# Kernel optimization log

Measured on AMD Instinct MI355X. Metric: run time of the kernel, lower is better.

## Reference

```python
import jax, jax.numpy as jnp
import numpy as np

B, N, D_IN, D_OUT, R = 8, 2048, 256, 256, 4


def setup_inputs() -> dict:
    key = jax.random.key(0)
    k1, k2, k3, k4 = jax.random.split(key, 4)
    x = jax.random.normal(k1, (B, N, D_IN), dtype=jnp.float32)
    adj = jnp.zeros((1,), dtype=jnp.float32)  # unused by the module
    # relation-type matrix: 0 = no edge, 1..R = relation id
    relation = jax.random.randint(k2, (B, N, N), 0, R + 1, dtype=jnp.int32)
    weight = jax.random.normal(k3, (R, D_IN, D_OUT), dtype=jnp.float32) * 0.05
    bias = jax.random.normal(k4, (D_OUT,), dtype=jnp.float32) * 0.05
    return {"x": x, "adj": adj, "relation": relation, "weight": weight, "bias": bias}


def reference(x, adj, relation, weight, bias):
    # Binary per-relation adjacency masks: [R, B, N, N]
    rel_ids = jnp.arange(1, weight.shape[0] + 1, dtype=relation.dtype)
    masks = (relation[None] == rel_ids[:, None, None, None]).astype(x.dtype)
    # Aggregate neighbors per relation: h[r] = A_r @ x  -> [R, B, N, D_in]
    h = jnp.einsum('rbnm,bmd->rbnd', masks, x)
    # Per-relation output transform, summed over relations: [B, N, D_out]
    y = jnp.einsum('rbnd,rdo->bno', h, weight)
    return y + bias
```

## Files before the change

kernel.cpp:

```cpp
#include <hip/hip_runtime.h>
#include <hip/hip_bf16.h>
#include <stdint.h>

typedef uint32_t u32;
typedef uint64_t u64;
typedef __bf16 bf16x8 __attribute__((ext_vector_type(8)));
typedef float f32x4 __attribute__((ext_vector_type(4)));
typedef u32 u32x4 __attribute__((ext_vector_type(4)));

#define NB 8
#define NN 2048
#define DIN 256
#define DOUT 256
#define NR 4
#define KTOT (NN * NR)

#define XW_BYTES   (NB * DOUT * KTOT * 2)
#define PART_BYTES (NB * NN * DOUT * 4)
#define WT_BYTES   (NR * DIN * DOUT * 2)
#define PART_ELEMS (NB * NN * DOUT)

__device__ __forceinline__ ushort f2bf(float f) {
  union { float f; u32 u; } c; c.f = f;
  return (ushort)((c.u + 0x7FFFu + ((c.u >> 16) & 1u)) >> 16);
}

__device__ __forceinline__ float bf2f(ushort u) {
  union { u32 i; float f; } c; c.i = ((u32)u) << 16; return c.f;
}

__device__ __forceinline__ void gload_lds16(const void* g, void* l) {
  __builtin_amdgcn_global_load_lds(
      (const __attribute__((address_space(1))) u32*)g,
      (__attribute__((address_space(3))) u32*)l, 16, 0, 0);
}

__global__ void k0_wT(const float* __restrict__ w, ushort* __restrict__ wT) {
  int i = blockIdx.x * 256 + threadIdx.x;
  int o = i & 255, d = (i >> 8) & 255, r = i >> 16;
  wT[(r * DOUT + o) * DIN + d] = f2bf(w[i]);
}

__global__ __launch_bounds__(512) void k1_xw(const float* __restrict__ x,
                                             const ushort* __restrict__ wT,
                                             ushort* __restrict__ xwT) {
  __shared__ char smem[73728];
  char* const Ab0 = smem;
  char* const Ab1 = smem + 4096;
  char* const Bb0 = smem + 8192;
  char* const Bb1 = smem + 40960;
  const int t = threadIdx.x, l = t & 63, w = t >> 6;
  const int r = w >> 1, oh = w & 1;
  const int blk = blockIdx.x;
  const int b = blk >> 6, rest = blk & 63, mc = rest >> 1, ot = rest & 1;

  f32x4 acc[4][4] = {};
  const int fr = l & 15, fq = l >> 4;
  const int ru = ((fq ^ (fr & 3)) << 4);

  const int arow = t >> 3;
  const int abyte = ((((t & 7) >> 1) ^ (arow & 3)) << 4) + (t & 1) * 8;
  const float* xg = x + ((size_t)(b * NN + mc * 64 + arow) * DIN + (t & 7) * 4);

  const int bdd = (((t & 3) ^ ((t >> 2) & 3)) << 3);
  const int bro = (t >> 2);

#define K1_GLDB(D0, BB)                                                        \
  {                                                                            \
    _Pragma("unroll") for (int i = 0; i < 4; ++i) {                            \
      const ushort* src = wT + ((size_t)(i * DOUT + ot * 128 + bro) * DIN +    \
                                (D0) + bdd);                                   \
      gload_lds16(src, (BB) + i * 8192 + t * 16);                              \
    }                                                                          \
  }

#define K1_WRA(AB, XV)                                                         \
  {                                                                            \
    ushort4 a4;                                                                \
    a4.x = f2bf((XV).x); a4.y = f2bf((XV).y);                                  \
    a4.z = f2bf((XV).z); a4.w = f2bf((XV).w);                                  \
    *(ushort4*)((AB) + arow * 64 + abyte) = a4;                                \
  }

#define K1_MFMA(AB, BB)                                                        \
  {                                                                            \
    bf16x8 af[4];                                                              \
    __builtin_amdgcn_s_setprio(1);                                             \
    _Pragma("unroll") for (int fm = 0; fm < 4; ++fm)                           \
      af[fm] = *(const bf16x8*)((AB) + (fm * 16 + fr) * 64 + ru);              \
    _Pragma("unroll") for (int fo = 0; fo < 4; ++fo) {                         \
      bf16x8 bf = *(const bf16x8*)((BB) + (size_t)(r * 128 + oh * 64 +         \
                                   fo * 16 + fr) * 64 + ru);                   \
      _Pragma("unroll") for (int fm = 0; fm < 4; ++fm)                         \
        acc[fm][fo] = __builtin_amdgcn_mfma_f32_16x16x32_bf16(                 \
            af[fm], bf, acc[fm][fo], 0, 0, 0);                                 \
    }                                                                          \
    __builtin_amdgcn_s_setprio(0);                                             \
  }

#define K1_ENDF()                                                              \
  asm volatile("s_waitcnt vmcnt(0) lgkmcnt(0)" ::: "memory");                  \
  __builtin_amdgcn_s_barrier();                                                \
  __builtin_amdgcn_sched_barrier(0);

#define K1_STEP(S, AP, BP, AQ, BQ)                                             \
  {                                                                            \
    K1_GLDB((S + 1) * 32, BQ);                                                 \
    __builtin_amdgcn_sched_barrier(0);                                         \
    float4 xv = *(const float4*)(xg + (S + 1) * 32);                           \
    K1_MFMA(AP, BP);                                                           \
    K1_WRA(AQ, xv);                                                            \
    K1_ENDF();                                                                 \
  }

  K1_GLDB(0, Bb0);
  __builtin_amdgcn_sched_barrier(0);
  {
    float4 xv = *(const float4*)(xg);
    K1_WRA(Ab0, xv);
  }
  K1_ENDF();

  K1_STEP(0, Ab0, Bb0, Ab1, Bb1);
  K1_STEP(1, Ab1, Bb1, Ab0, Bb0);
  K1_STEP(2, Ab0, Bb0, Ab1, Bb1);
  K1_STEP(3, Ab1, Bb1, Ab0, Bb0);
  K1_STEP(4, Ab0, Bb0, Ab1, Bb1);
  K1_STEP(5, Ab1, Bb1, Ab0, Bb0);
  K1_STEP(6, Ab0, Bb0, Ab1, Bb1);
  K1_MFMA(Ab1, Bb1);
  __syncthreads();

  ushort* Cs = (ushort*)smem;
#pragma unroll
  for (int fm = 0; fm < 4; ++fm)
#pragma unroll
    for (int fo = 0; fo < 4; ++fo)
#pragma unroll
      for (int j = 0; j < 4; ++j) {
        int o_loc = oh * 64 + fo * 16 + fr;
        int ml = fm * 16 + fq * 4 + j;
        Cs[o_loc * 256 + ml * 4 + r] = f2bf(acc[fm][fo][j]);
      }
  __syncthreads();
#pragma unroll
  for (int i = 0; i < 8; ++i) {
    int el = (i * 512 + t) * 8;
    int o_loc = el >> 8, kp = el & 255;
    *(uint4*)(xwT + (size_t)(b * DOUT + ot * 128 + o_loc) * KTOT + mc * 256 + kp) =
        *(const uint4*)(Cs + el);
  }
#undef K1_STEP
#undef K1_ENDF
#undef K1_MFMA
#undef K1_WRA
#undef K1_GLDB
}

__global__ __launch_bounds__(512, 2) void k2_v2(const int* __restrict__ rel,
                                                const ushort* __restrict__ xwT,
                                                ushort* __restrict__ partb) {
  __shared__ char smem[131072];
  const int t = threadIdx.x, l = t & 63, w = t >> 6;
  const int wm = w >> 2, wn = w & 3;
  const int logical = (blockIdx.x & 7) * 32 + (blockIdx.x >> 3);
  const int b = logical >> 5;
  const int nt = (logical >> 2) & 7;
  const int ks = logical & 3;

  f32x4 acc[8][4] = {};
  const int fr = l & 15, fq = l >> 4;
  const int rswz = (fr & 7) << 4;

  char* const Ab0 = smem;
  char* const Ab1 = smem + 32768;
  char* const Bb0 = smem + 65536;
  char* const Bb1 = smem + 98304;

  const int arow = t >> 1, half = t & 1;
  const int aswz = (arow & 7) << 4;
  const int* relg = rel + ((size_t)(b * NN + nt * 256 + arow)) * NN + ks * 512 + half * 8;

  const int brow = t >> 3;
  const int kd = (((t & 7) ^ ((t >> 3) & 7)) << 3);
  const ushort* xwb = xwT + (size_t)b * DOUT * KTOT + ks * 2048;

  int4 rs0a, rs0b, rs1a, rs1b;

#define GLD_ALL(S, BB)                                                         \
  {                                                                            \
    _Pragma("unroll") for (int i = 0; i < 4; ++i)                              \
      gload_lds16(xwb + (size_t)(brow + 64 * i) * KTOT + (S) * 64 + kd,        \
                  (BB) + i * 8192 + t * 16);                                   \
  }

#define RELLOAD(S, RA, RB)                                                     \
  RA = *(const int4*)(relg + (S) * 16);                                        \
  RB = *(const int4*)(relg + (S) * 16 + 4);

#define EXPAND_A(ABASE, V0, V1)                                                \
  {                                                                            \
    char* rowp = (ABASE) + arow * 128;                                         \
    int vv[8] = {V0.x, V0.y, V0.z, V0.w, V1.x, V1.y, V1.z, V1.w};              \
    _Pragma("unroll") for (int p = 0; p < 4; ++p) {                            \
      int va = vv[2 * p], vb = vv[2 * p + 1];                                  \
      u32 sa = ((u32)(va - 1) & 3u) * 16u;                                     \
      u32 sb = ((u32)(vb - 1) & 3u) * 16u;                                     \
      u64 ha = va ? (0x3F80ull << sa) : 0ull;                                  \
      u64 hb = vb ? (0x3F80ull << sb) : 0ull;                                  \
      u32x4 e = {(u32)ha, (u32)(ha >> 32), (u32)hb, (u32)(hb >> 32)};          \
      *(u32x4*)(rowp + ((half * 64 + p * 16) ^ aswz)) = e;                     \
    }                                                                          \
  }

#define RDB(BV, BB, KK)                                                        \
  _Pragma("unroll") for (int fo = 0; fo < 4; ++fo)                             \
    BV[fo] = *(const bf16x8*)((BB) + (wn * 64 + fo * 16 + fr) * 128 +          \
                              (((KK) * 64 + fq * 16) ^ rswz));

#define RDA(AV, AB, FM0, KK)                                                   \
  _Pragma("unroll") for (int i = 0; i < 4; ++i)                                \
    AV[i] = *(const bf16x8*)((AB) + (wm * 128 + ((FM0) + i) * 16 + fr) * 128 + \
                             (((KK) * 64 + fq * 16) ^ rswz));

#define MFMA4(FM0, AV, BV)                                                     \
  __builtin_amdgcn_s_setprio(1);                                               \
  _Pragma("unroll") for (int i = 0; i < 4; ++i)                                \
    _Pragma("unroll") for (int fo = 0; fo < 4; ++fo)                           \
      acc[(FM0) + i][fo] = __builtin_amdgcn_mfma_f32_16x16x32_bf16(            \
          AV[i], BV[fo], acc[(FM0) + i][fo], 0, 0, 0);                         \
  __builtin_amdgcn_s_setprio(0);

#define ENDFENCE(VMS)                                                          \
  asm volatile("s_waitcnt vmcnt(" VMS ") lgkmcnt(0)" ::: "memory");            \
  __builtin_amdgcn_s_barrier();                                                \
  __builtin_amdgcn_sched_barrier(0);

#define STEP(S, P, Q, STG, REL, EXP, VMS)                                      \
  {                                                                            \
    bf16x8 b0[4], b1[4], aA[4], aB[4], aC[4], aD[4];                           \
    RDB(b0, Bb##P, 0);                                                         \
    RDA(aA, Ab##P, 0, 0);                                                      \
    if (STG) { GLD_ALL((S) + 1, Bb##Q); }                                      \
    __builtin_amdgcn_sched_barrier(0);                                         \
    if (REL) { RELLOAD((S) + 2, rs##P##a, rs##P##b); }                         \
    RDA(aB, Ab##P, 4, 0);                                                      \
    MFMA4(0, aA, b0);                                                          \
    RDA(aC, Ab##P, 0, 1);                                                      \
    if (EXP) { EXPAND_A(Ab##Q, rs##Q##a, rs##Q##b); }                          \
    MFMA4(4, aB, b0);                                                          \
    RDB(b1, Bb##P, 1);                                                         \
    RDA(aD, Ab##P, 4, 1);                                                      \
    MFMA4(0, aC, b1);                                                          \
    MFMA4(4, aD, b1);                                                          \
    ENDFENCE(VMS);                                                             \
  }

  GLD_ALL(0, Bb0);
  __builtin_amdgcn_sched_barrier(0);
  RELLOAD(0, rs0a, rs0b);
  RELLOAD(1, rs1a, rs1b);
  EXPAND_A(Ab0, rs0a, rs0b);
  ENDFENCE("4");

  for (int s = 0; s < 30; s += 2) {
    STEP(s, 0, 1, 1, 1, 1, "2");
    STEP(s + 1, 1, 0, 1, 1, 1, "2");
  }
  STEP(30, 0, 1, 1, 0, 1, "0");
  {
    bf16x8 b0[4], b1[4], aA[4], aB[4], aC[4], aD[4];
    RDB(b0, Bb1, 0);
    RDA(aA, Ab1, 0, 0);
    RDA(aB, Ab1, 4, 0);
    MFMA4(0, aA, b0);
    RDA(aC, Ab1, 0, 1);
    MFMA4(4, aB, b0);
    RDB(b1, Bb1, 1);
    RDA(aD, Ab1, 4, 1);
    MFMA4(0, aC, b1);
    MFMA4(4, aD, b1);
  }

  ushort* dst = partb + (size_t)ks * PART_ELEMS;
#pragma unroll
  for (int fm = 0; fm < 8; ++fm)
#pragma unroll
    for (int fo = 0; fo < 4; ++fo) {
      int n = nt * 256 + wm * 128 + fm * 16 + fq * 4;
      int o = wn * 64 + fo * 16 + fr;
#pragma unroll
      for (int j = 0; j < 4; ++j)
        dst[(size_t)(b * NN + n + j) * DOUT + o] = f2bf(acc[fm][fo][j]);
    }
#undef STEP
#undef ENDFENCE
#undef MFMA4
#undef RDA
#undef RDB
#undef EXPAND_A
#undef RELLOAD
#undef GLD_ALL
}

__global__ void k3_sum(float* __restrict__ out, const ushort* __restrict__ partb,
                       const float* __restrict__ bias) {
  int i = blockIdx.x * 256 + threadIdx.x;
  float4 s = ((const float4*)bias)[i & 63];
#pragma unroll
  for (int p = 0; p < 4; ++p) {
    ushort4 v = ((const ushort4*)(partb + (size_t)p * PART_ELEMS))[i];
    s.x += bf2f(v.x); s.y += bf2f(v.y); s.z += bf2f(v.z); s.w += bf2f(v.w);
  }
  ((float4*)out)[i] = s;
}

__global__ __launch_bounds__(256, 2) void k2_r4(const int* __restrict__ rel,
                                                const ushort* __restrict__ xwT,
                                                float* __restrict__ out,
                                                float* __restrict__ part) {
  __shared__ char smem[81920];
  const int t = threadIdx.x, l = t & 63, w = t >> 6;
  const int wr = w >> 1, wc = w & 1;
  const int logical = (blockIdx.x & 7) * 64 + (blockIdx.x >> 3);
  const int b = logical >> 6;
  const int nt = (logical >> 2) & 15;
  const int ks = (logical >> 1) & 1;
  const int ot = logical & 1;

  f32x4 acc[4][4] = {};
  const int arow = t >> 1, half = t & 1;
  const int* relg = rel + ((size_t)(b * NN + nt * 128 + arow) * NN + ks * 1024 + half * 8);
  const ushort* xwb = xwT + (size_t)(b * DOUT + ot * 128) * KTOT + ks * 4096;

  char* const Ab0 = smem;
  char* const Ab1 = smem + 16384;
  char* const Bb0 = smem + 32768;
  char* const Bb1 = smem + 49152;
  char* const Bb2 = smem + 65536;

  const int brow = t >> 3;
  const int kd = (((t & 7) ^ ((t >> 3) & 7)) << 3);
  const int aswz = (arow & 7) << 4;
  const int fr = l & 15, fq = l >> 4;
  const int rswz = (fr & 7) << 4;

  int4 rsA0, rsB0, rsA1, rsB1;

#define STAGE_B(S, BBASE)                                                      \
  {                                                                            \
    _Pragma("unroll") for (int i = 0; i < 4; ++i)                              \
      gload_lds16(xwb + (size_t)(brow + 32 * i) * KTOT + (S) * 64 + kd,        \
                  (BBASE) + i * 4096 + t * 16);                                \
  }
#define RELLOAD(S, RA, RB)                                                     \
  RA = *(const int4*)(relg + (S) * 16);                                        \
  RB = *(const int4*)(relg + (S) * 16 + 4);
#define EXPAND_A(ABASE, V0, V1)                                                \
  {                                                                            \
    char* rowp = (ABASE) + arow * 128;                                         \
    int vv[8] = {V0.x, V0.y, V0.z, V0.w, V1.x, V1.y, V1.z, V1.w};              \
    _Pragma("unroll") for (int p = 0; p < 4; ++p) {                            \
      int va = vv[2 * p], vb = vv[2 * p + 1];                                  \
      u32 sa = ((u32)(va - 1) & 3u) * 16u;                                     \
      u32 sb = ((u32)(vb - 1) & 3u) * 16u;                                     \
      u64 ha = va ? (0x3F80ull << sa) : 0ull;                                  \
      u64 hb = vb ? (0x3F80ull << sb) : 0ull;                                  \
      u32x4 e = {(u32)ha, (u32)(ha >> 32), (u32)hb, (u32)(hb >> 32)};          \
      *(u32x4*)(rowp + ((half * 64 + p * 16) ^ aswz)) = e;                     \
    }                                                                          \
  }
#define BARV6()                                                                \
  asm volatile("s_waitcnt vmcnt(6) lgkmcnt(0)" ::: "memory");                  \
  __builtin_amdgcn_s_barrier();                                                \
  __builtin_amdgcn_sched_barrier(0);
#define BARV0()                                                                \
  asm volatile("s_waitcnt vmcnt(0) lgkmcnt(0)" ::: "memory");                  \
  __builtin_amdgcn_s_barrier();                                                \
  __builtin_amdgcn_sched_barrier(0);
#define MFMA_STEP(AC, BC)                                                      \
  __builtin_amdgcn_s_setprio(1);                                               \
  _Pragma("unroll") for (int kk = 0; kk < 2; ++kk) {                           \
    bf16x8 af[4], bfv[4];                                                      \
    const int colb = (kk * 64 + fq * 16) ^ rswz;                               \
    _Pragma("unroll") for (int fm = 0; fm < 4; ++fm)                           \
      af[fm] = *(const bf16x8*)((AC) + (wr * 64 + fm * 16 + fr) * 128 + colb); \
    _Pragma("unroll") for (int fo = 0; fo < 4; ++fo)                           \
      bfv[fo] = *(const bf16x8*)((BC) + (wc * 64 + fo * 16 + fr) * 128 + colb);\
    _Pragma("unroll") for (int fm = 0; fm < 4; ++fm)                           \
      _Pragma("unroll") for (int fo = 0; fo < 4; ++fo)                         \
        acc[fm][fo] = __builtin_amdgcn_mfma_f32_16x16x32_bf16(                 \
            af[fm], bfv[fo], acc[fm][fo], 0, 0, 0);                            \
  }                                                                            \
  __builtin_amdgcn_s_setprio(0);
#define BODY(S, ACUR, BCUR, ANXT, RLA, RLB, RCA, RCB, BSTG)                    \
  {                                                                            \
    STAGE_B((S) + 2, BSTG);                                                    \
    RELLOAD((S) + 2, RLA, RLB);                                                \
    MFMA_STEP(ACUR, BCUR);                                                     \
    EXPAND_A(ANXT, RCA, RCB);                                                  \
    BARV6();                                                                   \
  }

  STAGE_B(0, Bb0);
  RELLOAD(0, rsA0, rsB0);
  STAGE_B(1, Bb1);
  RELLOAD(1, rsA1, rsB1);
  EXPAND_A(Ab0, rsA0, rsB0);
  BARV6();

  for (int s = 0; s < 60; s += 6) {
    BODY(s + 0, Ab0, Bb0, Ab1, rsA0, rsB0, rsA1, rsB1, Bb2);
    BODY(s + 1, Ab1, Bb1, Ab0, rsA1, rsB1, rsA0, rsB0, Bb0);
    BODY(s + 2, Ab0, Bb2, Ab1, rsA0, rsB0, rsA1, rsB1, Bb1);
    BODY(s + 3, Ab1, Bb0, Ab0, rsA1, rsB1, rsA0, rsB0, Bb2);
    BODY(s + 4, Ab0, Bb1, Ab1, rsA0, rsB0, rsA1, rsB1, Bb0);
    BODY(s + 5, Ab1, Bb2, Ab0, rsA1, rsB1, rsA0, rsB0, Bb1);
  }
  BODY(60, Ab0, Bb0, Ab1, rsA0, rsB0, rsA1, rsB1, Bb2);
  BODY(61, Ab1, Bb1, Ab0, rsA1, rsB1, rsA0, rsB0, Bb0);
  {
    MFMA_STEP(Ab0, Bb2);
    EXPAND_A(Ab1, rsA1, rsB1);
    BARV0();
  }
  {
    MFMA_STEP(Ab1, Bb0);
  }

  float* dst = ks ? part : out;
#pragma unroll
  for (int fm = 0; fm < 4; ++fm)
#pragma unroll
    for (int fo = 0; fo < 4; ++fo) {
      int n = nt * 128 + wr * 64 + fm * 16 + fq * 4;
      int o = ot * 128 + wc * 64 + fo * 16 + fr;
#pragma unroll
      for (int j = 0; j < 4; ++j)
        dst[(size_t)(b * NN + n + j) * DOUT + o] = acc[fm][fo][j];
    }
#undef BODY
#undef MFMA_STEP
#undef BARV6
#undef BARV0
#undef EXPAND_A
#undef RELLOAD
#undef STAGE_B
}

__global__ void k3_r4(float* __restrict__ out, const float* __restrict__ part,
                      const float* __restrict__ bias) {
  int i = blockIdx.x * 256 + threadIdx.x;
  float4 o = ((const float4*)out)[i];
  float4 p = ((const float4*)part)[i];
  float4 bv = ((const float4*)bias)[i & 63];
  float4 rr;
  rr.x = o.x + p.x + bv.x;
  rr.y = o.y + p.y + bv.y;
  rr.z = o.z + p.z + bv.z;
  rr.w = o.w + p.w + bv.w;
  ((float4*)out)[i] = rr;
}

extern "C" void kernel_launch(void* const* d_in, const int* in_sizes, int n_in,
                              void* d_out, int out_size, void* d_ws, size_t ws_size,
                              hipStream_t stream) {
  const float* x = (const float*)d_in[0];
  const int* rel = (const int*)d_in[2];
  const float* wgt = (const float*)d_in[3];
  const float* bias = (const float*)d_in[4];
  float* out = (float*)d_out;
  char* ws = (char*)d_ws;

  const size_t partb_bytes = (size_t)PART_ELEMS * 2 * 4;
  const size_t need_big = (size_t)XW_BYTES + partb_bytes + WT_BYTES;
  if (ws_size >= need_big) {
    ushort* xwT = (ushort*)ws;
    ushort* partb = (ushort*)(ws + XW_BYTES);
    ushort* wT = (ushort*)(ws + XW_BYTES + partb_bytes);
    k0_wT<<<1024, 256, 0, stream>>>(wgt, wT);
    k1_xw<<<512, 512, 0, stream>>>(x, wT, xwT);
    k2_v2<<<256, 512, 0, stream>>>(rel, xwT, partb);
    k3_sum<<<4096, 256, 0, stream>>>(out, partb, bias);
  } else {
    ushort* xwT = (ushort*)ws;
    float* part = (float*)(ws + XW_BYTES);
    ushort* wT = (ushort*)(ws + XW_BYTES + PART_BYTES);
    k0_wT<<<1024, 256, 0, stream>>>(wgt, wT);
    k1_xw<<<512, 512, 0, stream>>>(x, wT, xwT);
    k2_r4<<<512, 256, 0, stream>>>(rel, xwT, out, part);
    k3_r4<<<4096, 256, 0, stream>>>(out, part, bias);
  }
}
```

Measured before the change: 108.4 us.

## Retile relation GEMM to 256x128 tiles with 32-wide K steps for higher occupancy

The main aggregation kernel is retiled. Each block now computes a 256-row by 128-column output tile instead of 256x256, and the K step shrinks from 64 to 32, so LDS per block drops from 128KB to 48KB. The grid doubles to 512 blocks with launch bounds allowing 4 blocks per CU, and the LDS swizzle is redone for 64-byte rows. The aim is more resident waves and better latency hiding. The cost is that the relation matrix is read and expanded twice (once per output half), and there are twice as many barriers per unit of K.

```diff
diff --git a/kernel.cpp b/kernel.cpp
--- a/kernel.cpp
+++ b/kernel.cpp
@@ -157,150 +157,133 @@
 #undef K1_GLDB
 }
 
-__global__ __launch_bounds__(512, 2) void k2_v2(const int* __restrict__ rel,
+__global__ __launch_bounds__(512, 4) void k2_v7(const int* __restrict__ rel,
                                                 const ushort* __restrict__ xwT,
                                                 ushort* __restrict__ partb) {
-  __shared__ char smem[131072];
+  __shared__ char smem[49152];
   const int t = threadIdx.x, l = t & 63, w = t >> 6;
-  const int wm = w >> 2, wn = w & 3;
-  const int logical = (blockIdx.x & 7) * 32 + (blockIdx.x >> 3);
-  const int b = logical >> 5;
-  const int nt = (logical >> 2) & 7;
+  const int wm = w >> 1, wn = w & 1;
+  const int logical = (blockIdx.x & 7) * 64 + (blockIdx.x >> 3);
+  const int b = logical >> 6;
+  const int nt = (logical >> 3) & 7;
+  const int ot = (logical >> 2) & 1;
   const int ks = logical & 3;
 
-  f32x4 acc[8][4] = {};
+  f32x4 acc[4][4] = {};
   const int fr = l & 15, fq = l >> 4;
-  const int rswz = (fr & 7) << 4;
+  const int runit = ((fq ^ (fr & 3) ^ ((fr >> 2) & 3)) << 4);
 
   char* const Ab0 = smem;
-  char* const Ab1 = smem + 32768;
-  char* const Bb0 = smem + 65536;
-  char* const Bb1 = smem + 98304;
+  char* const Ab1 = smem + 16384;
+  char* const Bb0 = smem + 32768;
+  char* const Bb1 = smem + 40960;
 
   const int arow = t >> 1, half = t & 1;
-  const int aswz = (arow & 7) << 4;
-  const int* relg = rel + ((size_t)(b * NN + nt * 256 + arow)) * NN + ks * 512 + half * 8;
-
-  const int brow = t >> 3;
-  const int kd = (((t & 7) ^ ((t >> 3) & 7)) << 3);
-  const ushort* xwb = xwT + (size_t)b * DOUT * KTOT + ks * 2048;
-
-  int4 rs0a, rs0b, rs1a, rs1b;
-
-#define GLD_ALL(S, BB)                                                         \
-  {                                                                            \
-    _Pragma("unroll") for (int i = 0; i < 4; ++i)                              \
-      gload_lds16(xwb + (size_t)(brow + 64 * i) * KTOT + (S) * 64 + kd,        \
-                  (BB) + i * 8192 + t * 16);                                   \
-  }
-
-#define RELLOAD(S, RA, RB)                                                     \
-  RA = *(const int4*)(relg + (S) * 16);                                        \
-  RB = *(const int4*)(relg + (S) * 16 + 4);
-
-#define EXPAND_A(ABASE, V0, V1)                                                \
-  {                                                                            \
-    char* rowp = (ABASE) + arow * 128;                                         \
-    int vv[8] = {V0.x, V0.y, V0.z, V0.w, V1.x, V1.y, V1.z, V1.w};              \
-    _Pragma("unroll") for (int p = 0; p < 4; ++p) {                            \
-      int va = vv[2 * p], vb = vv[2 * p + 1];                                  \
-      u32 sa = ((u32)(va - 1) & 3u) * 16u;                                     \
-      u32 sb = ((u32)(vb - 1) & 3u) * 16u;                                     \
-      u64 ha = va ? (0x3F80ull << sa) : 0ull;                                  \
-      u64 hb = vb ? (0x3F80ull << sb) : 0ull;                                  \
-      u32x4 e = {(u32)ha, (u32)(ha >> 32), (u32)hb, (u32)(hb >> 32)};          \
-      *(u32x4*)(rowp + ((half * 64 + p * 16) ^ aswz)) = e;                     \
-    }                                                                          \
-  }
-
-#define RDB(BV, BB, KK)                                                        \
+  const int* relg = rel + ((size_t)(b * NN + nt * 256 + arow)) * NN + ks * 512 + half * 4;
+  const u32 awz = ((u32)arow & 3u) ^ (((u32)arow >> 2) & 3u);
+  char* const rowA0 = Ab0 + arow * 64;
+  char* const rowA1 = Ab1 + arow * 64;
+
+  const int brow = t >> 2;
+  const int bsw = (((t & 3) ^ ((brow & 3) ^ ((brow >> 2) & 3))) << 3);
+  const ushort* xwb = xwT + (size_t)(b * DOUT + ot * 128) * KTOT + ks * 2048;
+
+  int4 rs0, rs1;
+
+#define GLD_B(S, BB)                                                           \
+  gload_lds16(xwb + (size_t)brow * KTOT + (S) * 32 + bsw, (BB) + t * 16);
+
+#define RELLOAD(S, R) R = *(const int4*)(relg + (S) * 8);
+
+#define EXPROW(ROWP, V)                                                        \
+  {                                                                            \
+    u32 sa = ((u32)((V).x - 1) & 3u) * 16u, sb = ((u32)((V).y - 1) & 3u) * 16u;\
+    u32 sc = ((u32)((V).z - 1) & 3u) * 16u, sd = ((u32)((V).w - 1) & 3u) * 16u;\
+    u64 ha = (V).x ? (0x3F80ull << sa) : 0ull;                                 \
+    u64 hb = (V).y ? (0x3F80ull << sb) : 0ull;                                 \
+    u64 hc = (V).z ? (0x3F80ull << sc) : 0ull;                                 \
+    u64 hd = (V).w ? (0x3F80ull << sd) : 0ull;                                 \
+    u32x4 e0 = {(u32)ha, (u32)(ha >> 32), (u32)hb, (u32)(hb >> 32)};           \
+    u32x4 e1 = {(u32)hc, (u32)(hc >> 32), (u32)hd, (u32)(hd >> 32)};           \
+    *(u32x4*)((ROWP) + ((((u32)(half * 2 + 0)) ^ awz) << 4)) = e0;             \
+    *(u32x4*)((ROWP) + ((((u32)(half * 2 + 1)) ^ awz) << 4)) = e1;             \
+  }
+
+#define RDA(AV, AB)                                                            \
+  _Pragma("unroll") for (int fm = 0; fm < 4; ++fm)                             \
+    AV[fm] = *(const bf16x8*)((AB) + (wm * 64 + fm * 16 + fr) * 64 + runit);
+
+#define RDB(BV, BB)                                                            \
   _Pragma("unroll") for (int fo = 0; fo < 4; ++fo)                             \
-    BV[fo] = *(const bf16x8*)((BB) + (wn * 64 + fo * 16 + fr) * 128 +          \
-                              (((KK) * 64 + fq * 16) ^ rswz));
-
-#define RDA(AV, AB, FM0, KK)                                                   \
-  _Pragma("unroll") for (int i = 0; i < 4; ++i)                                \
-    AV[i] = *(const bf16x8*)((AB) + (wm * 128 + ((FM0) + i) * 16 + fr) * 128 + \
-                             (((KK) * 64 + fq * 16) ^ rswz));
-
-#define MFMA4(FM0, AV, BV)                                                     \
+    BV[fo] = *(const bf16x8*)((BB) + (wn * 64 + fo * 16 + fr) * 64 + runit);
+
+#define MFMA2(FM0, AV, BV)                                                     \
   __builtin_amdgcn_s_setprio(1);                                               \
-  _Pragma("unroll") for (int i = 0; i < 4; ++i)                                \
+  _Pragma("unroll") for (int i = 0; i < 2; ++i)                                \
     _Pragma("unroll") for (int fo = 0; fo < 4; ++fo)                           \
       acc[(FM0) + i][fo] = __builtin_amdgcn_mfma_f32_16x16x32_bf16(            \
-          AV[i], BV[fo], acc[(FM0) + i][fo], 0, 0, 0);                         \
+          AV[(FM0) + i], BV[fo], acc[(FM0) + i][fo], 0, 0, 0);                 \
   __builtin_amdgcn_s_setprio(0);
 
-#define ENDFENCE(VMS)                                                          \
+#define ENDF(VMS)                                                              \
   asm volatile("s_waitcnt vmcnt(" VMS ") lgkmcnt(0)" ::: "memory");            \
   __builtin_amdgcn_s_barrier();                                                \
   __builtin_amdgcn_sched_barrier(0);
 
 #define STEP(S, P, Q, STG, REL, EXP, VMS)                                      \
   {                                                                            \
-    bf16x8 b0[4], b1[4], aA[4], aB[4], aC[4], aD[4];                           \
-    RDB(b0, Bb##P, 0);                                                         \
-    RDA(aA, Ab##P, 0, 0);                                                      \
-    if (STG) { GLD_ALL((S) + 1, Bb##Q); }                                      \
+    bf16x8 av[4], bv[4];                                                       \
+    RDB(bv, Bb##P);                                                            \
+    RDA(av, Ab##P);                                                            \
+    if (STG) { GLD_B((S) + 1, Bb##Q); }                                        \
     __builtin_amdgcn_sched_barrier(0);                                         \
-    if (REL) { RELLOAD((S) + 2, rs##P##a, rs##P##b); }                         \
-    RDA(aB, Ab##P, 4, 0);                                                      \
-    MFMA4(0, aA, b0);                                                          \
-    RDA(aC, Ab##P, 0, 1);                                                      \
-    if (EXP) { EXPAND_A(Ab##Q, rs##Q##a, rs##Q##b); }                          \
-    MFMA4(4, aB, b0);                                                          \
-    RDB(b1, Bb##P, 1);                                                         \
-    RDA(aD, Ab##P, 4, 1);                                                      \
-    MFMA4(0, aC, b1);                                                          \
-    MFMA4(4, aD, b1);                                                          \
-    ENDFENCE(VMS);                                                             \
-  }
-
-  GLD_ALL(0, Bb0);
-  __builtin_amdgcn_sched_barrier(0);
-  RELLOAD(0, rs0a, rs0b);
-  RELLOAD(1, rs1a, rs1b);
-  EXPAND_A(Ab0, rs0a, rs0b);
-  ENDFENCE("4");
-
-  for (int s = 0; s < 30; s += 2) {
-    STEP(s, 0, 1, 1, 1, 1, "2");
-    STEP(s + 1, 1, 0, 1, 1, 1, "2");
-  }
-  STEP(30, 0, 1, 1, 0, 1, "0");
+    if (REL) { RELLOAD((S) + 2, rs##P); }                                      \
+    __builtin_amdgcn_sched_barrier(0);                                         \
+    MFMA2(0, av, bv);                                                          \
+    if (EXP) { EXPROW(rowA##Q, rs##Q); }                                       \
+    MFMA2(2, av, bv);                                                          \
+    ENDF(VMS);                                                                 \
+  }
+
+  GLD_B(0, Bb0);
+  __builtin_amdgcn_sched_barrier(0);
+  RELLOAD(0, rs0);
+  RELLOAD(1, rs1);
+  EXPROW(rowA0, rs0);
+  ENDF("1");
+
+  for (int s = 0; s < 62; s += 2) {
+    STEP(s, 0, 1, 1, 1, 1, "1");
+    STEP(s + 1, 1, 0, 1, 1, 1, "1");
+  }
+  STEP(62, 0, 1, 1, 0, 1, "0");
   {
-    bf16x8 b0[4], b1[4], aA[4], aB[4], aC[4], aD[4];
-    RDB(b0, Bb1, 0);
-    RDA(aA, Ab1, 0, 0);
-    RDA(aB, Ab1, 4, 0);
-    MFMA4(0, aA, b0);
-    RDA(aC, Ab1, 0, 1);
-    MFMA4(4, aB, b0);
-    RDB(b1, Bb1, 1);
-    RDA(aD, Ab1, 4, 1);
-    MFMA4(0, aC, b1);
-    MFMA4(4, aD, b1);
+    bf16x8 av[4], bv[4];
+    RDB(bv, Bb1);
+    RDA(av, Ab1);
+    MFMA2(0, av, bv);
+    MFMA2(2, av, bv);
   }
 
   ushort* dst = partb + (size_t)ks * PART_ELEMS;
 #pragma unroll
-  for (int fm = 0; fm < 8; ++fm)
+  for (int fm = 0; fm < 4; ++fm)
 #pragma unroll
     for (int fo = 0; fo < 4; ++fo) {
-      int n = nt * 256 + wm * 128 + fm * 16 + fq * 4;
-      int o = wn * 64 + fo * 16 + fr;
+      int n = nt * 256 + wm * 64 + fm * 16 + fq * 4;
+      int o = ot * 128 + wn * 64 + fo * 16 + fr;
 #pragma unroll
       for (int j = 0; j < 4; ++j)
         dst[(size_t)(b * NN + n + j) * DOUT + o] = f2bf(acc[fm][fo][j]);
     }
 #undef STEP
-#undef ENDFENCE
-#undef MFMA4
+#undef ENDF
+#undef MFMA2
+#undef RDB
 #undef RDA
-#undef RDB
-#undef EXPAND_A
+#undef EXPROW
 #undef RELLOAD
-#undef GLD_ALL
+#undef GLD_B
 }
 
 __global__ void k3_sum(float* __restrict__ out, const ushort* __restrict__ partb,
@@ -480,7 +463,7 @@
     ushort* wT = (ushort*)(ws + XW_BYTES + partb_bytes);
     k0_wT<<<1024, 256, 0, stream>>>(wgt, wT);
     k1_xw<<<512, 512, 0, stream>>>(x, wT, xwT);
-    k2_v2<<<256, 512, 0, stream>>>(rel, xwT, partb);
+    k2_v7<<<512, 512, 0, stream>>>(rel, xwT, partb);
     k3_sum<<<4096, 256, 0, stream>>>(out, partb, bias);
   } else {
     ushort* xwT = (ushort*)ws;
```

After: 122.5 us. +12.9%, slower.
